# Kernel optimization log

Hardware: AMD Instinct MI355X
Metric: run time of the kernel (lower is better)

## Reference

```python
import jax, jax.numpy as jnp
import numpy as np

N_RID, N_CELL, N_COLS, E, D_IN, D_H = 100000, 400000, 4, 100000, 64, 64


def _sage_gcn(feat_src, feat_dst, src, dst, W, b):
    # DGL SAGEConv, aggregator_type='gcn':
    #   h = (segment_sum(feat_src[src] -> dst) + feat_dst) / (in_deg + 1)
    #   out = h @ W + b   (no fc_self for 'gcn')
    n_dst = feat_dst.shape[0]
    msg = feat_src[src]                                   # [E, d] gather
    agg = jax.ops.segment_sum(msg, dst, num_segments=n_dst)
    deg = jax.ops.segment_sum(jnp.ones_like(dst, dtype=feat_src.dtype), dst,
                              num_segments=n_dst)
    h = (agg + feat_dst) / (deg + 1.0)[:, None]
    return h @ W + b


def setup_inputs() -> dict:
    key = jax.random.key(0)
    ks = jax.random.split(key, 16)
    inp = {
        "x_rid": jax.random.normal(ks[0], (N_RID, D_IN), jnp.float32),
        "x_cell": jax.random.normal(ks[1], (N_CELL, D_IN), jnp.float32),
        "src_fwd": jax.random.randint(ks[2], (N_COLS, E), 0, N_RID, jnp.int32),
        "dst_fwd": jax.random.randint(ks[3], (N_COLS, E), 0, N_CELL, jnp.int32),
        "src_rev": jax.random.randint(ks[4], (N_COLS, E), 0, N_CELL, jnp.int32),
        "dst_rev": jax.random.randint(ks[5], (N_COLS, E), 0, N_RID, jnp.int32),
        # layer-1 SAGEConv weights, one per relation (col: rid->cell, i_col: cell->rid)
        "W1f": jax.random.normal(ks[6], (N_COLS, D_IN, D_H), jnp.float32) / np.sqrt(D_IN),
        "b1f": jnp.zeros((N_COLS, D_H), jnp.float32),
        "W1r": jax.random.normal(ks[7], (N_COLS, D_IN, D_H), jnp.float32) / np.sqrt(D_IN),
        "b1r": jnp.zeros((N_COLS, D_H), jnp.float32),
        # layer-2 (inner) SAGEConv weights
        "W2f": jax.random.normal(ks[8], (N_COLS, D_H, D_H), jnp.float32) / np.sqrt(D_H),
        "b2f": jnp.zeros((N_COLS, D_H), jnp.float32),
        "W2r": jax.random.normal(ks[9], (N_COLS, D_H, D_H), jnp.float32) / np.sqrt(D_H),
        "b2r": jnp.zeros((N_COLS, D_H), jnp.float32),
    }
    return inp


def reference(x_rid, x_cell, src_fwd, dst_fwd, src_rev, dst_rev,
              W1f, b1f, W1r, b1r, W2f, b2f, W2r, b2r):
    sage_v = jax.vmap(_sage_gcn, in_axes=(None, None, 0, 0, 0, 0))

    def hetero_layer(h_rid, h_cell, Wf, bf, Wr, br):
        # HeteroGraphConv(aggregate='mean'): per dst node type, mean over relations
        cell = sage_v(h_rid, h_cell, src_fwd, dst_fwd, Wf, bf).mean(axis=0)
        rid = sage_v(h_cell, h_rid, src_rev, dst_rev, Wr, br).mean(axis=0)
        return rid, cell

    center = lambda x: x - jnp.mean(x, axis=0)

    rid, cell = hetero_layer(x_rid, x_cell, W1f, b1f, W1r, b1r)
    rid, cell = center(rid), center(cell)
    rid, cell = hetero_layer(rid, cell, W2f, b2f, W2r, b2r)
    rid, cell = center(rid), center(cell)

    h1 = cell.at[:rid.shape[0], :].set(rid)  # overwrite first n_rid cell rows
    return jax.nn.relu(h1)
```

## Files before the change

### kernel.cpp

```cpp
#include <hip/hip_runtime.h>

#define N_RID  100000
#define N_CELL 400000
#define NCOLS  4
#define NE     100000
#define D      64
#define TOTE   (NCOLS * NE)
#define TILE   64
#define NBF    (NCOLS * N_CELL)
#define NBR    (NCOLS * N_RID)
#define NCHF   ((NBF + 1023) / 1024)
#define NCHR   ((NBR + 1023) / 1024)
#define PST    68

typedef __attribute__((ext_vector_type(8))) short bf16x8;
typedef __attribute__((ext_vector_type(4))) float f32x4;

__device__ inline unsigned short f2bf(float f) {
    unsigned int u = __float_as_uint(f);
    return (unsigned short)((u + 0x7FFF + ((u >> 16) & 1)) >> 16);
}
__device__ inline float bf2f(unsigned short b) {
    return __uint_as_float(((unsigned int)b) << 16);
}
__device__ inline unsigned int cvtpk(float a, float b) {
    unsigned int r;
    asm("v_cvt_pk_bf16_f32 %0, %1, %2" : "=v"(r) : "v"(a), "v"(b));
    return r;
}
__device__ inline int swz(int row, int kbyte) {
    return row * 128 + (kbyte ^ ((row & 7) << 4));
}
__device__ inline void ldrow16(const unsigned short* h, size_t row, int q,
                               float4& a, float4& b) {
    bf16x8 r = *(const bf16x8*)(h + row * D + q * 8);
    a.x = bf2f((unsigned short)r[0]); a.y = bf2f((unsigned short)r[1]);
    a.z = bf2f((unsigned short)r[2]); a.w = bf2f((unsigned short)r[3]);
    b.x = bf2f((unsigned short)r[4]); b.y = bf2f((unsigned short)r[5]);
    b.z = bf2f((unsigned short)r[6]); b.w = bf2f((unsigned short)r[7]);
}

__global__ void hist2(const int* __restrict__ dstF, const int* __restrict__ dstR,
                      int* __restrict__ cntF, int* __restrict__ cntR) {
    int t = blockIdx.x * 256 + threadIdx.x;
    if (t < TOTE) {
        int c = t / NE;
        atomicAdd(&cntF[c * N_CELL + dstF[t]], 1);
    } else if (t < 2 * TOTE) {
        int t2 = t - TOTE;
        int c = t2 / NE;
        atomicAdd(&cntR[c * N_RID + dstR[t2]], 1);
    }
}

__global__ void scan1_2(const int* __restrict__ inF, int* __restrict__ outF,
                        int* __restrict__ csF, const int* __restrict__ inR,
                        int* __restrict__ outR, int* __restrict__ csR) {
    __shared__ int lds[256];
    const int b = blockIdx.x;
    const int* in; int* outp; int* cs; int n, bb;
    if (b < NCHF) { in = inF; outp = outF; cs = csF; n = NBF; bb = b; }
    else          { in = inR; outp = outR; cs = csR; n = NBR; bb = b - NCHF; }
    int base = bb * 1024 + threadIdx.x * 4;
    int v0 = 0, v1 = 0, v2 = 0, v3 = 0;
    if (base + 0 < n) v0 = in[base + 0];
    if (base + 1 < n) v1 = in[base + 1];
    if (base + 2 < n) v2 = in[base + 2];
    if (base + 3 < n) v3 = in[base + 3];
    int tsum = v0 + v1 + v2 + v3;
    lds[threadIdx.x] = tsum;
    __syncthreads();
    for (int off = 1; off < 256; off <<= 1) {
        int x = (threadIdx.x >= off) ? lds[threadIdx.x - off] : 0;
        __syncthreads();
        lds[threadIdx.x] += x;
        __syncthreads();
    }
    int excl = lds[threadIdx.x] - tsum;
    if (base + 0 < n) outp[base + 0] = excl;
    if (base + 1 < n) outp[base + 1] = excl + v0;
    if (base + 2 < n) outp[base + 2] = excl + v0 + v1;
    if (base + 3 < n) outp[base + 3] = excl + v0 + v1 + v2;
    if (threadIdx.x == 255) cs[bb] = lds[255];
}

__global__ void scan2_2(int* __restrict__ aF, int* __restrict__ aR) {
    __shared__ int lds[256];
    int* a = blockIdx.x ? aR : aF;
    int m  = blockIdx.x ? NCHR : NCHF;
    int per = (m + 255) >> 8;
    int st = threadIdx.x * per;
    int s = 0;
    for (int i = 0; i < per; ++i) if (st + i < m) s += a[st + i];
    lds[threadIdx.x] = s;
    __syncthreads();
    for (int off = 1; off < 256; off <<= 1) {
        int x = (threadIdx.x >= off) ? lds[threadIdx.x - off] : 0;
        __syncthreads();
        lds[threadIdx.x] += x;
        __syncthreads();
    }
    int run = lds[threadIdx.x] - s;
    for (int i = 0; i < per; ++i) if (st + i < m) { int v = a[st + i]; a[st + i] = run; run += v; }
}

__global__ void scan3_2(int* __restrict__ outF, const int* __restrict__ csF,
                        int* __restrict__ outR, const int* __restrict__ csR) {
    const int gF = (NBF + 255) / 256;
    int b = blockIdx.x;
    if (b == 0 && threadIdx.x == 0) { outF[NBF] = TOTE; outR[NBR] = TOTE; }
    if (b < gF) {
        int i = b * 256 + threadIdx.x;
        if (i < NBF) outF[i] += csF[i >> 10];
    } else {
        int i = (b - gF) * 256 + threadIdx.x;
        if (i < NBR) outR[i] += csR[i >> 10];
    }
}

__global__ void fill2(const int* __restrict__ dstF, const int* __restrict__ srcF,
                      const int* __restrict__ ptrF, int* __restrict__ cntF,
                      int* __restrict__ colF,
                      const int* __restrict__ dstR, const int* __restrict__ srcR,
                      const int* __restrict__ ptrR, int* __restrict__ cntR,
                      int* __restrict__ colR) {
    int t = blockIdx.x * 256 + threadIdx.x;
    if (t < TOTE) {
        int c = t / NE;
        int bin = c * N_CELL + dstF[t];
        int old = atomicSub(&cntF[bin], 1);
        colF[ptrF[bin] + old - 1] = srcF[t];
    } else if (t < 2 * TOTE) {
        int t2 = t - TOTE;
        int c = t2 / NE;
        int bin = c * N_RID + dstR[t2];
        int old = atomicSub(&cntR[bin], 1);
        colR[ptrR[bin] + old - 1] = srcR[t2];
    }
}

__global__ void prep_w(const float* __restrict__ Wa, const float* __restrict__ Wb,
                       const float* __restrict__ Wc, const float* __restrict__ Wd,
                       unsigned short* __restrict__ Ta, unsigned short* __restrict__ Tb,
                       unsigned short* __restrict__ Tc, unsigned short* __restrict__ Td) {
    int t = blockIdx.x * 256 + threadIdx.x;
    if (t >= NCOLS * D * D) return;
    int c = t >> 12, jk = t & 4095, j = jk >> 6, k = jk & 63;
    int s = (c * D + k) * D + j;
    Ta[t] = f2bf(Wa[s]);
    Tb[t] = f2bf(Wb[s]);
    Tc[t] = f2bf(Wc[s]);
    Td[t] = f2bf(Wd[s]);
}

__global__ void prep_x(const float* __restrict__ xr, const float* __restrict__ xc,
                       unsigned short* __restrict__ xr16,
                       unsigned short* __restrict__ xc16) {
    const int NR = N_RID * D / 8;
    const int NC = N_CELL * D / 8;
    int t = blockIdx.x * 256 + threadIdx.x;
    if (t >= NR + NC) return;
    const float4* src; unsigned short* dst; size_t i;
    if (t < NR) { i = (size_t)t;       src = (const float4*)xr; dst = xr16; }
    else        { i = (size_t)t - NR;  src = (const float4*)xc; dst = xc16; }
    float4 a = src[2 * i], b = src[2 * i + 1];
    int4 st;
    st.x = (int)cvtpk(a.x, a.y); st.y = (int)cvtpk(a.z, a.w);
    st.z = (int)cvtpk(b.x, b.y); st.w = (int)cvtpk(b.z, b.w);
    *(int4*)(dst + i * 8) = st;
}

template<bool OUTBF>
__global__ void __launch_bounds__(256, 4) sage2(
        const unsigned short* __restrict__ hdC, const unsigned short* __restrict__ hsC,
        const int* __restrict__ ptrC, const int* __restrict__ colC,
        const unsigned short* __restrict__ WtC, const float* __restrict__ biasC,
        const float* __restrict__ mudC, const float* __restrict__ musC,
        void* __restrict__ outC, float* __restrict__ csC,
        const unsigned short* __restrict__ hdR, const unsigned short* __restrict__ hsR,
        const int* __restrict__ ptrR, const int* __restrict__ colR,
        const unsigned short* __restrict__ WtR, const float* __restrict__ biasR,
        const float* __restrict__ mudR, const float* __restrict__ musR,
        void* __restrict__ outR, float* __restrict__ csR, int gC) {
    __shared__ int pl[NCOLS][TILE + 1];
    __shared__ __align__(16) float stage[4][16 * PST];

    const int tid = threadIdx.x, w = tid >> 6, l = tid & 63;
    const int g = l >> 3, q = l & 7;

    const bool rrole = (int)blockIdx.x >= gC;
    const unsigned short* h_dst = rrole ? hdR : hdC;
    const unsigned short* h_src = rrole ? hsR : hsC;
    const int* ptr    = rrole ? ptrR : ptrC;
    const int* col    = rrole ? colR : colC;
    const unsigned short* Wt = rrole ? WtR : WtC;
    const float* bias = rrole ? biasR : biasC;
    const float* mu_d = rrole ? mudR : mudC;
    const float* mu_s = rrole ? musR : musC;
    void* out   = rrole ? outR : outC;
    float* csum = rrole ? csR : csC;
    const int n_dst = rrole ? N_RID : N_CELL;
    const int row0 = (rrole ? (int)blockIdx.x - gC : (int)blockIdx.x) * TILE;

    unsigned short* aHi = (unsigned short*)stage[w];
    unsigned short* aLo = aHi + 1024;
    float* pw = stage[w];

    for (int i = tid; i < NCOLS * (TILE + 1); i += 256) {
        int cc = i / (TILE + 1), r = i % (TILE + 1);
        pl[cc][r] = ptr[(size_t)cc * n_dst + min(row0 + r, n_dst)];
    }

    float4 t0[NCOLS][2], t1[NCOLS][2];
#pragma unroll
    for (int i = 0; i < 2; ++i) {
        int re = min(row0 + w * 16 + i * 8 + g, n_dst - 1);
        float4 v0, v1;
        ldrow16(h_dst, (size_t)re, q, v0, v1);
        if (mu_d) {
            float4 m0 = ((const float4*)mu_d)[2 * q], m1 = ((const float4*)mu_d)[2 * q + 1];
            v0.x -= m0.x; v0.y -= m0.y; v0.z -= m0.z; v0.w -= m0.w;
            v1.x -= m1.x; v1.y -= m1.y; v1.z -= m1.z; v1.w -= m1.w;
        }
#pragma unroll
        for (int c = 0; c < NCOLS; ++c) { t0[c][i] = v0; t1[c][i] = v1; }
    }
    float4 ms0 = {0, 0, 0, 0}, ms1 = {0, 0, 0, 0};
    if (mu_s) { ms0 = ((const float4*)mu_s)[2 * q]; ms1 = ((const float4*)mu_s)[2 * q + 1]; }
    const int j0 = l & 15;
    float bbv[4];
#pragma unroll
    for (int nt = 0; nt < 4; ++nt)
        bbv[nt] = 0.25f * (bias[nt * 16 + j0] + bias[64 + nt * 16 + j0] +
                           bias[128 + nt * 16 + j0] + bias[192 + nt * 16 + j0]);
    __syncthreads();

#pragma unroll
    for (int c = 0; c < NCOLS; ++c)
#pragma unroll
        for (int i = 0; i < 2; ++i) {
            int r = w * 16 + i * 8 + g;
            int p0 = pl[c][r], p1 = pl[c][r + 1];
            for (int e = p0; e < p1; ++e) {
                float4 u0, u1;
                ldrow16(h_src, (size_t)col[e], q, u0, u1);
                t0[c][i].x += u0.x; t0[c][i].y += u0.y;
                t0[c][i].z += u0.z; t0[c][i].w += u0.w;
                t1[c][i].x += u1.x; t1[c][i].y += u1.y;
                t1[c][i].z += u1.z; t1[c][i].w += u1.w;
            }
        }

    f32x4 macc[4] = {};
#pragma unroll
    for (int c = 0; c < NCOLS; ++c) {
#pragma unroll
        for (int i = 0; i < 2; ++i) {
            int rloc = i * 8 + g;
            int row = w * 16 + rloc;
            float dg = (float)(pl[c][row + 1] - pl[c][row]);
            float scv = 1.0f / (dg + 1.0f);
            float4 a = t0[c][i], b = t1[c][i];
            a.x = (a.x - dg * ms0.x) * scv; a.y = (a.y - dg * ms0.y) * scv;
            a.z = (a.z - dg * ms0.z) * scv; a.w = (a.w - dg * ms0.w) * scv;
            b.x = (b.x - dg * ms1.x) * scv; b.y = (b.y - dg * ms1.y) * scv;
            b.z = (b.z - dg * ms1.z) * scv; b.w = (b.w - dg * ms1.w) * scv;
            unsigned int h01 = cvtpk(a.x, a.y), h23 = cvtpk(a.z, a.w);
            unsigned int h45 = cvtpk(b.x, b.y), h67 = cvtpk(b.z, b.w);
            float r0 = a.x - __uint_as_float(h01 << 16);
            float r1 = a.y - __uint_as_float(h01 & 0xFFFF0000u);
            float r2 = a.z - __uint_as_float(h23 << 16);
            float r3 = a.w - __uint_as_float(h23 & 0xFFFF0000u);
            float r4 = b.x - __uint_as_float(h45 << 16);
            float r5 = b.y - __uint_as_float(h45 & 0xFFFF0000u);
            float r6 = b.z - __uint_as_float(h67 << 16);
            float r7 = b.w - __uint_as_float(h67 & 0xFFFF0000u);
            unsigned int l01 = cvtpk(r0, r1), l23 = cvtpk(r2, r3);
            unsigned int l45 = cvtpk(r4, r5), l67 = cvtpk(r6, r7);
            int off = swz(rloc, q * 16);
            *(unsigned long long*)((char*)aHi + off) =
                (unsigned long long)h01 | ((unsigned long long)h23 << 32);
            *(unsigned long long*)((char*)aHi + off + 8) =
                (unsigned long long)h45 | ((unsigned long long)h67 << 32);
            *(unsigned long long*)((char*)aLo + off) =
                (unsigned long long)l01 | ((unsigned long long)l23 << 32);
            *(unsigned long long*)((char*)aLo + off + 8) =
                (unsigned long long)l45 | ((unsigned long long)l67 << 32);
        }
        bf16x8 wf[4][2];
#pragma unroll
        for (int nt = 0; nt < 4; ++nt) {
            const unsigned short* wb = Wt + ((c * D + nt * 16 + (l & 15)) * D + (l >> 4) * 8);
            wf[nt][0] = *(const bf16x8*)(wb);
            wf[nt][1] = *(const bf16x8*)(wb + 32);
        }
        bf16x8 ah[2], al[2];
#pragma unroll
        for (int kh = 0; kh < 2; ++kh) {
            int off = swz(l & 15, kh * 64 + (l >> 4) * 16);
            ah[kh] = *(const bf16x8*)((const char*)aHi + off);
            al[kh] = *(const bf16x8*)((const char*)aLo + off);
        }
        __builtin_amdgcn_s_setprio(1);
#pragma unroll
        for (int nt = 0; nt < 4; ++nt) {
            macc[nt] = __builtin_amdgcn_mfma_f32_16x16x32_bf16(ah[0], wf[nt][0], macc[nt], 0, 0, 0);
            macc[nt] = __builtin_amdgcn_mfma_f32_16x16x32_bf16(ah[1], wf[nt][1], macc[nt], 0, 0, 0);
            macc[nt] = __builtin_amdgcn_mfma_f32_16x16x32_bf16(al[0], wf[nt][0], macc[nt], 0, 0, 0);
            macc[nt] = __builtin_amdgcn_mfma_f32_16x16x32_bf16(al[1], wf[nt][1], macc[nt], 0, 0, 0);
        }
        __builtin_amdgcn_s_setprio(0);
    }

    float cs[4] = {0.f, 0.f, 0.f, 0.f};
#pragma unroll
    for (int nt = 0; nt < 4; ++nt)
#pragma unroll
        for (int qq = 0; qq < 4; ++qq) {
            int rl = (l >> 4) * 4 + qq;
            float v = 0.25f * macc[nt][qq] + bbv[nt];
            pw[rl * PST + nt * 16 + j0] = v;
            if (row0 + w * 16 + rl < n_dst) cs[nt] += v;
        }
    if (OUTBF) {
#pragma unroll
        for (int it = 0; it < 2; ++it) {
            int e = it * 512 + l * 8;
            int rl = e >> 6, c0 = e & 63;
            int grow = row0 + w * 16 + rl;
            float4 a = *(const float4*)&pw[rl * PST + c0];
            float4 b = *(const float4*)&pw[rl * PST + c0 + 4];
            int4 st;
            st.x = (int)cvtpk(a.x, a.y); st.y = (int)cvtpk(a.z, a.w);
            st.z = (int)cvtpk(b.x, b.y); st.w = (int)cvtpk(b.z, b.w);
            if (grow < n_dst)
                *(int4*)((unsigned short*)out + (size_t)grow * D + c0) = st;
        }
    } else {
#pragma unroll
        for (int it = 0; it < 4; ++it) {
            int idx = it * 64 + l;
            int rl = idx >> 4, c4 = (idx & 15) * 4;
            int grow = row0 + w * 16 + rl;
            float4 v = *(const float4*)&pw[rl * PST + c4];
            if (grow < n_dst)
                *(float4*)((float*)out + (size_t)grow * D + c4) = v;
        }
    }
#pragma unroll
    for (int nt = 0; nt < 4; ++nt) {
        float v = cs[nt];
        v += __shfl_xor(v, 16);
        v += __shfl_xor(v, 32);
        if (l < 16) atomicAdd(&csum[(blockIdx.x & 63) * 64 + nt * 16 + l], v);
    }
}

__global__ void finalize2(const float* __restrict__ repA, float* __restrict__ muA,
                          float invA, const float* __restrict__ repB,
                          float* __restrict__ muB, float invB) {
    int j = threadIdx.x;
    const float* rep = blockIdx.x ? repB : repA;
    float* mu        = blockIdx.x ? muB : muA;
    float inv        = blockIdx.x ? invB : invA;
    float s = 0.f;
    for (int k = 0; k < 64; ++k) s += rep[k * 64 + j];
    mu[j] = s * inv;
}

__global__ void final_combine(float* __restrict__ out, const float* __restrict__ rid,
        const float* __restrict__ mu_c, const float* __restrict__ mu_r) {
    int t = blockIdx.x * 256 + threadIdx.x;
    if (t >= N_CELL * D) return;
    int row = t >> 6, j = t & 63;
    float v = (row < N_RID) ? (rid[(size_t)row * D + j] - mu_r[j])
                            : (out[t] - mu_c[j]);
    out[t] = fmaxf(v, 0.0f);
}

extern "C" void kernel_launch(void* const* d_in, const int* in_sizes, int n_in,
                              void* d_out, int out_size, void* d_ws, size_t ws_size,
                              hipStream_t stream) {
    const float* x_rid  = (const float*)d_in[0];
    const float* x_cell = (const float*)d_in[1];
    const int* src_fwd  = (const int*)d_in[2];
    const int* dst_fwd  = (const int*)d_in[3];
    const int* src_rev  = (const int*)d_in[4];
    const int* dst_rev  = (const int*)d_in[5];
    const float* W1f = (const float*)d_in[6];
    const float* b1f = (const float*)d_in[7];
    const float* W1r = (const float*)d_in[8];
    const float* b1r = (const float*)d_in[9];
    const float* W2f = (const float*)d_in[10];
    const float* b2f = (const float*)d_in[11];
    const float* W2r = (const float*)d_in[12];
    const float* b2r = (const float*)d_in[13];
    float* out = (float*)d_out;

    char* p = (char*)d_ws;
    float* rid2 = (float*)p;                     p += (size_t)N_RID * D * 4;
    unsigned short* cell1 = (unsigned short*)p;  p += (size_t)N_CELL * D * 2;
    unsigned short* rid1  = (unsigned short*)p;  p += (size_t)N_RID * D * 2;
    unsigned short* xr16  = (unsigned short*)p;  p += (size_t)N_RID * D * 2;
    unsigned short* xc16  = (unsigned short*)p;  p += (size_t)N_CELL * D * 2;
    float* csums = (float*)p;                    p += (size_t)4 * 4096 * 4;
    float* mus   = (float*)p;                    p += 4 * 64 * 4;
    int* ptrF = (int*)p;                         p += (size_t)(NBF + 4) * 4;
    int* colF = (int*)p;                         p += (size_t)TOTE * 4;
    int* ptrR = (int*)p;                         p += (size_t)(NBR + 4) * 4;
    int* colR = (int*)p;                         p += (size_t)TOTE * 4;
    unsigned short* Wt1f = (unsigned short*)p;   p += NCOLS * D * D * 2;
    unsigned short* Wt1r = (unsigned short*)p;   p += NCOLS * D * D * 2;
    unsigned short* Wt2f = (unsigned short*)p;   p += NCOLS * D * D * 2;
    unsigned short* Wt2r = (unsigned short*)p;   p += NCOLS * D * D * 2;
    int* cntF  = (int*)rid2;
    int* cntR  = cntF + NBF;
    int* csumF = cntR + NBR;
    int* csumR = csumF + 2048;

    float* cs_c1 = csums;
    float* cs_r1 = csums + 4096;
    float* cs_o  = csums + 8192;
    float* cs_r2 = csums + 12288;
    float* mu_c1 = mus;
    float* mu_r1 = mus + 64;
    float* mu_o  = mus + 128;
    float* mu_r2 = mus + 192;

    hipMemsetAsync(cntF, 0, (size_t)(NBF + NBR) * sizeof(int), stream);
    hipMemsetAsync(csums, 0, (size_t)4 * 4096 * sizeof(float), stream);

    prep_w<<<(NCOLS * D * D + 255) / 256, 256, 0, stream>>>(W1f, W1r, W2f, W2r,
                                                            Wt1f, Wt1r, Wt2f, Wt2r);
    const int gx = ((N_RID + N_CELL) * D / 8 + 255) / 256;
    prep_x<<<gx, 256, 0, stream>>>(x_rid, x_cell, xr16, xc16);

    const int g2e = (2 * TOTE + 255) / 256;
    hist2<<<g2e, 256, 0, stream>>>(dst_fwd, dst_rev, cntF, cntR);
    scan1_2<<<NCHF + NCHR, 256, 0, stream>>>(cntF, ptrF, csumF, cntR, ptrR, csumR);
    scan2_2<<<2, 256, 0, stream>>>(csumF, csumR);
    scan3_2<<<(NBF + 255) / 256 + (NBR + 255) / 256, 256, 0, stream>>>(ptrF, csumF,
                                                                       ptrR, csumR);
    fill2<<<g2e, 256, 0, stream>>>(dst_fwd, src_fwd, ptrF, cntF, colF,
                                   dst_rev, src_rev, ptrR, cntR, colR);

    const int gC = N_CELL / TILE;
    const int gR = (N_RID + TILE - 1) / TILE;

    sage2<true><<<gC + gR, 256, 0, stream>>>(
        xc16, xr16, ptrF, colF, Wt1f, b1f, nullptr, nullptr, cell1, cs_c1,
        xr16, xc16, ptrR, colR, Wt1r, b1r, nullptr, nullptr, rid1, cs_r1, gC);
    finalize2<<<2, 64, 0, stream>>>(cs_c1, mu_c1, 1.0f / N_CELL,
                                    cs_r1, mu_r1, 1.0f / N_RID);

    sage2<false><<<gC + gR, 256, 0, stream>>>(
        cell1, rid1, ptrF, colF, Wt2f, b2f, mu_c1, mu_r1, out, cs_o,
        rid1, cell1, ptrR, colR, Wt2r, b2r, mu_r1, mu_c1, rid2, cs_r2, gC);
    finalize2<<<2, 64, 0, stream>>>(cs_o, mu_o, 1.0f / N_CELL,
                                    cs_r2, mu_r2, 1.0f / N_RID);

    final_combine<<<(N_CELL * D) / 256, 256, 0, stream>>>(out, rid2, mu_o, mu_r2);
}
```

Before: 533.6 us.

## Remap sage2 gather to 4 lanes per row and stage edge indices in LDS

Each destination row is now handled by 4 lanes reading 32 bytes each (16 bf16 features) instead of 8 lanes of 16 bytes, covering all 16 rows per wave in a single pass. Each relation's aggregation is also moved inside the per-relation MMA loop, so fewer accumulators stay live at once. The first ECOL column indices of every relation's edge range are preloaded into shared memory, and the centering means are held in LDS. The aim is more independent gathers in flight, lower register pressure and fewer dependent global index loads, at the cost of more LDS and an extra barrier.

```diff
diff --git a/kernel.cpp b/kernel.cpp
--- a/kernel.cpp
+++ b/kernel.cpp
@@ -12,6 +12,7 @@
 #define NCHF   ((NBF + 1023) / 1024)
 #define NCHR   ((NBR + 1023) / 1024)
 #define PST    68
+#define ECOL   128
 
 typedef __attribute__((ext_vector_type(8))) short bf16x8;
 typedef __attribute__((ext_vector_type(4))) float f32x4;
@@ -30,14 +31,6 @@
 }
 __device__ inline int swz(int row, int kbyte) {
     return row * 128 + (kbyte ^ ((row & 7) << 4));
-}
-__device__ inline void ldrow16(const unsigned short* h, size_t row, int q,
-                               float4& a, float4& b) {
-    bf16x8 r = *(const bf16x8*)(h + row * D + q * 8);
-    a.x = bf2f((unsigned short)r[0]); a.y = bf2f((unsigned short)r[1]);
-    a.z = bf2f((unsigned short)r[2]); a.w = bf2f((unsigned short)r[3]);
-    b.x = bf2f((unsigned short)r[4]); b.y = bf2f((unsigned short)r[5]);
-    b.z = bf2f((unsigned short)r[6]); b.w = bf2f((unsigned short)r[7]);
 }
 
 __global__ void hist2(const int* __restrict__ dstF, const int* __restrict__ dstR,
@@ -183,10 +176,12 @@
         const float* __restrict__ mudR, const float* __restrict__ musR,
         void* __restrict__ outR, float* __restrict__ csR, int gC) {
     __shared__ int pl[NCOLS][TILE + 1];
+    __shared__ int ecol[NCOLS][ECOL];
+    __shared__ float mudL[64], musL[64];
     __shared__ __align__(16) float stage[4][16 * PST];
 
     const int tid = threadIdx.x, w = tid >> 6, l = tid & 63;
-    const int g = l >> 3, q = l & 7;
+    const int g16 = l >> 2, q4 = l & 3;
 
     const bool rrole = (int)blockIdx.x >= gC;
     const unsigned short* h_dst = rrole ? hdR : hdC;
@@ -210,23 +205,39 @@
         int cc = i / (TILE + 1), r = i % (TILE + 1);
         pl[cc][r] = ptr[(size_t)cc * n_dst + min(row0 + r, n_dst)];
     }
-
-    float4 t0[NCOLS][2], t1[NCOLS][2];
-#pragma unroll
-    for (int i = 0; i < 2; ++i) {
-        int re = min(row0 + w * 16 + i * 8 + g, n_dst - 1);
-        float4 v0, v1;
-        ldrow16(h_dst, (size_t)re, q, v0, v1);
-        if (mu_d) {
-            float4 m0 = ((const float4*)mu_d)[2 * q], m1 = ((const float4*)mu_d)[2 * q + 1];
-            v0.x -= m0.x; v0.y -= m0.y; v0.z -= m0.z; v0.w -= m0.w;
-            v1.x -= m1.x; v1.y -= m1.y; v1.z -= m1.z; v1.w -= m1.w;
-        }
-#pragma unroll
-        for (int c = 0; c < NCOLS; ++c) { t0[c][i] = v0; t1[c][i] = v1; }
-    }
-    float4 ms0 = {0, 0, 0, 0}, ms1 = {0, 0, 0, 0};
-    if (mu_s) { ms0 = ((const float4*)mu_s)[2 * q]; ms1 = ((const float4*)mu_s)[2 * q + 1]; }
+    if (tid < 64)            mudL[tid]      = mu_d ? mu_d[tid]      : 0.f;
+    else if (tid < 128)      musL[tid - 64] = mu_s ? mu_s[tid - 64] : 0.f;
+    __syncthreads();
+
+#pragma unroll
+    for (int c = 0; c < NCOLS; ++c) {
+        int eb = pl[c][0];
+        int len = min(pl[c][TILE] - eb, ECOL);
+        for (int i = tid; i < len; i += 256) ecol[c][i] = col[eb + i];
+    }
+
+    float4 s0, s1, s2, s3;
+    {
+        int re = min(row0 + w * 16 + g16, n_dst - 1);
+        const unsigned short* sp = h_dst + (size_t)re * D + q4 * 16;
+        bf16x8 u0 = *(const bf16x8*)sp;
+        bf16x8 u1 = *(const bf16x8*)(sp + 8);
+        const float4* md = (const float4*)&mudL[q4 * 16];
+        float4 m0 = md[0], m1 = md[1], m2 = md[2], m3 = md[3];
+        s0.x = bf2f((unsigned short)u0[0]) - m0.x; s0.y = bf2f((unsigned short)u0[1]) - m0.y;
+        s0.z = bf2f((unsigned short)u0[2]) - m0.z; s0.w = bf2f((unsigned short)u0[3]) - m0.w;
+        s1.x = bf2f((unsigned short)u0[4]) - m1.x; s1.y = bf2f((unsigned short)u0[5]) - m1.y;
+        s1.z = bf2f((unsigned short)u0[6]) - m1.z; s1.w = bf2f((unsigned short)u0[7]) - m1.w;
+        s2.x = bf2f((unsigned short)u1[0]) - m2.x; s2.y = bf2f((unsigned short)u1[1]) - m2.y;
+        s2.z = bf2f((unsigned short)u1[2]) - m2.z; s2.w = bf2f((unsigned short)u1[3]) - m2.w;
+        s3.x = bf2f((unsigned short)u1[4]) - m3.x; s3.y = bf2f((unsigned short)u1[5]) - m3.y;
+        s3.z = bf2f((unsigned short)u1[6]) - m3.z; s3.w = bf2f((unsigned short)u1[7]) - m3.w;
+    }
+    float4 ms0, ms1, ms2, ms3;
+    {
+        const float4* ms = (const float4*)&musL[q4 * 16];
+        ms0 = ms[0]; ms1 = ms[1]; ms2 = ms[2]; ms3 = ms[3];
+    }
     const int j0 = l & 15;
     float bbv[4];
 #pragma unroll
@@ -235,57 +246,69 @@
                            bias[128 + nt * 16 + j0] + bias[192 + nt * 16 + j0]);
     __syncthreads();
 
-#pragma unroll
-    for (int c = 0; c < NCOLS; ++c)
-#pragma unroll
-        for (int i = 0; i < 2; ++i) {
-            int r = w * 16 + i * 8 + g;
-            int p0 = pl[c][r], p1 = pl[c][r + 1];
-            for (int e = p0; e < p1; ++e) {
-                float4 u0, u1;
-                ldrow16(h_src, (size_t)col[e], q, u0, u1);
-                t0[c][i].x += u0.x; t0[c][i].y += u0.y;
-                t0[c][i].z += u0.z; t0[c][i].w += u0.w;
-                t1[c][i].x += u1.x; t1[c][i].y += u1.y;
-                t1[c][i].z += u1.z; t1[c][i].w += u1.w;
-            }
-        }
-
     f32x4 macc[4] = {};
 #pragma unroll
     for (int c = 0; c < NCOLS; ++c) {
-#pragma unroll
-        for (int i = 0; i < 2; ++i) {
-            int rloc = i * 8 + g;
-            int row = w * 16 + rloc;
-            float dg = (float)(pl[c][row + 1] - pl[c][row]);
-            float scv = 1.0f / (dg + 1.0f);
-            float4 a = t0[c][i], b = t1[c][i];
-            a.x = (a.x - dg * ms0.x) * scv; a.y = (a.y - dg * ms0.y) * scv;
-            a.z = (a.z - dg * ms0.z) * scv; a.w = (a.w - dg * ms0.w) * scv;
-            b.x = (b.x - dg * ms1.x) * scv; b.y = (b.y - dg * ms1.y) * scv;
-            b.z = (b.z - dg * ms1.z) * scv; b.w = (b.w - dg * ms1.w) * scv;
-            unsigned int h01 = cvtpk(a.x, a.y), h23 = cvtpk(a.z, a.w);
-            unsigned int h45 = cvtpk(b.x, b.y), h67 = cvtpk(b.z, b.w);
-            float r0 = a.x - __uint_as_float(h01 << 16);
-            float r1 = a.y - __uint_as_float(h01 & 0xFFFF0000u);
-            float r2 = a.z - __uint_as_float(h23 << 16);
-            float r3 = a.w - __uint_as_float(h23 & 0xFFFF0000u);
-            float r4 = b.x - __uint_as_float(h45 << 16);
-            float r5 = b.y - __uint_as_float(h45 & 0xFFFF0000u);
-            float r6 = b.z - __uint_as_float(h67 << 16);
-            float r7 = b.w - __uint_as_float(h67 & 0xFFFF0000u);
-            unsigned int l01 = cvtpk(r0, r1), l23 = cvtpk(r2, r3);
-            unsigned int l45 = cvtpk(r4, r5), l67 = cvtpk(r6, r7);
-            int off = swz(rloc, q * 16);
-            *(unsigned long long*)((char*)aHi + off) =
-                (unsigned long long)h01 | ((unsigned long long)h23 << 32);
-            *(unsigned long long*)((char*)aHi + off + 8) =
-                (unsigned long long)h45 | ((unsigned long long)h67 << 32);
-            *(unsigned long long*)((char*)aLo + off) =
-                (unsigned long long)l01 | ((unsigned long long)l23 << 32);
-            *(unsigned long long*)((char*)aLo + off + 8) =
-                (unsigned long long)l45 | ((unsigned long long)l67 << 32);
+        int p0 = pl[c][w * 16 + g16], p1 = pl[c][w * 16 + g16 + 1];
+        int eb = pl[c][0];
+        float4 a0 = s0, a1 = s1, a2 = s2, a3 = s3;
+        for (int e = p0; e < p1; ++e) {
+            int idx = e - eb;
+            int v = (idx < ECOL) ? ecol[c][idx] : col[e];
+            const unsigned short* rp = h_src + (size_t)v * D + q4 * 16;
+            bf16x8 u0 = *(const bf16x8*)rp;
+            bf16x8 u1 = *(const bf16x8*)(rp + 8);
+            a0.x += bf2f((unsigned short)u0[0]); a0.y += bf2f((unsigned short)u0[1]);
+            a0.z += bf2f((unsigned short)u0[2]); a0.w += bf2f((unsigned short)u0[3]);
+            a1.x += bf2f((unsigned short)u0[4]); a1.y += bf2f((unsigned short)u0[5]);
+            a1.z += bf2f((unsigned short)u0[6]); a1.w += bf2f((unsigned short)u0[7]);
+            a2.x += bf2f((unsigned short)u1[0]); a2.y += bf2f((unsigned short)u1[1]);
+            a2.z += bf2f((unsigned short)u1[2]); a2.w += bf2f((unsigned short)u1[3]);
+            a3.x += bf2f((unsigned short)u1[4]); a3.y += bf2f((unsigned short)u1[5]);
+            a3.z += bf2f((unsigned short)u1[6]); a3.w += bf2f((unsigned short)u1[7]);
+        }
+        float dg = (float)(p1 - p0);
+        float scv = 1.0f / (dg + 1.0f);
+        a0.x = (a0.x - dg * ms0.x) * scv; a0.y = (a0.y - dg * ms0.y) * scv;
+        a0.z = (a0.z - dg * ms0.z) * scv; a0.w = (a0.w - dg * ms0.w) * scv;
+        a1.x = (a1.x - dg * ms1.x) * scv; a1.y = (a1.y - dg * ms1.y) * scv;
+        a1.z = (a1.z - dg * ms1.z) * scv; a1.w = (a1.w - dg * ms1.w) * scv;
+        a2.x = (a2.x - dg * ms2.x) * scv; a2.y = (a2.y - dg * ms2.y) * scv;
+        a2.z = (a2.z - dg * ms2.z) * scv; a2.w = (a2.w - dg * ms2.w) * scv;
+        a3.x = (a3.x - dg * ms3.x) * scv; a3.y = (a3.y - dg * ms3.y) * scv;
+        a3.z = (a3.z - dg * ms3.z) * scv; a3.w = (a3.w - dg * ms3.w) * scv;
+        {
+            unsigned int h0 = cvtpk(a0.x, a0.y), h1 = cvtpk(a0.z, a0.w);
+            unsigned int h2 = cvtpk(a1.x, a1.y), h3 = cvtpk(a1.z, a1.w);
+            unsigned int h4 = cvtpk(a2.x, a2.y), h5 = cvtpk(a2.z, a2.w);
+            unsigned int h6 = cvtpk(a3.x, a3.y), h7 = cvtpk(a3.z, a3.w);
+            float r0 = a0.x - __uint_as_float(h0 << 16);
+            float r1 = a0.y - __uint_as_float(h0 & 0xFFFF0000u);
+            float r2 = a0.z - __uint_as_float(h1 << 16);
+            float r3 = a0.w - __uint_as_float(h1 & 0xFFFF0000u);
+            float r4 = a1.x - __uint_as_float(h2 << 16);
+            float r5 = a1.y - __uint_as_float(h2 & 0xFFFF0000u);
+            float r6 = a1.z - __uint_as_float(h3 << 16);
+            float r7 = a1.w - __uint_as_float(h3 & 0xFFFF0000u);
+            float r8 = a2.x - __uint_as_float(h4 << 16);
+            float r9 = a2.y - __uint_as_float(h4 & 0xFFFF0000u);
+            float rA = a2.z - __uint_as_float(h5 << 16);
+            float rB = a2.w - __uint_as_float(h5 & 0xFFFF0000u);
+            float rC = a3.x - __uint_as_float(h6 << 16);
+            float rD = a3.y - __uint_as_float(h6 & 0xFFFF0000u);
+            float rE = a3.z - __uint_as_float(h7 << 16);
+            float rF = a3.w - __uint_as_float(h7 & 0xFFFF0000u);
+            int4 hiA; hiA.x = (int)h0; hiA.y = (int)h1; hiA.z = (int)h2; hiA.w = (int)h3;
+            int4 hiB; hiB.x = (int)h4; hiB.y = (int)h5; hiB.z = (int)h6; hiB.w = (int)h7;
+            int4 loA; loA.x = (int)cvtpk(r0, r1); loA.y = (int)cvtpk(r2, r3);
+            loA.z = (int)cvtpk(r4, r5); loA.w = (int)cvtpk(r6, r7);
+            int4 loB; loB.x = (int)cvtpk(r8, r9); loB.y = (int)cvtpk(rA, rB);
+            loB.z = (int)cvtpk(rC, rD); loB.w = (int)cvtpk(rE, rF);
+            int offA = swz(g16, q4 * 32), offB = swz(g16, q4 * 32 + 16);
+            *(int4*)((char*)aHi + offA) = hiA;
+            *(int4*)((char*)aHi + offB) = hiB;
+            *(int4*)((char*)aLo + offA) = loA;
+            *(int4*)((char*)aLo + offB) = loB;
         }
         bf16x8 wf[4][2];
 #pragma unroll
```

Result: faster. 480.9 us (-9.9%).
